# Performance work log

Measured on AMD Instinct MI355X. Metric: run time of the kernel, lower is better.

Reference implementation:

```python
import jax, jax.numpy as jnp
import numpy as np

N_HEAD = 16
ROPE_THETA = 10000.0


def setup_inputs() -> dict:
    key = jax.random.key(0)
    k0, k1, k2 = jax.random.split(key, 3)
    B, T, C = 2, 2048, 1024
    s = 0.02  # GPT-2 style init scale
    return {
        "x": jax.random.normal(k0, (B, T, C), jnp.float32),
        "w_attn": jax.random.normal(k1, (C, 3 * C), jnp.float32) * s,
        "b_attn": jnp.zeros((3 * C,), jnp.float32),
        "w_proj": jax.random.normal(k2, (C, C), jnp.float32) * s,
        "b_proj": jnp.zeros((C,), jnp.float32),
    }


def _rope(x):
    # x: [B, H, T, D]; interleaved-pair rotary (lucidrains rotate_queries_or_keys)
    T, D = x.shape[-2], x.shape[-1]
    inv_freq = 1.0 / (ROPE_THETA ** (jnp.arange(0, D, 2, dtype=jnp.float32) / D))
    freqs = jnp.arange(T, dtype=jnp.float32)[:, None] * inv_freq[None, :]  # [T, D/2]
    emb = jnp.repeat(freqs, 2, axis=-1)  # [T, D], each freq duplicated per pair
    cos, sin = jnp.cos(emb), jnp.sin(emb)
    xr = x.reshape(*x.shape[:-1], D // 2, 2)
    x1, x2 = xr[..., 0], xr[..., 1]
    rot = jnp.stack((-x2, x1), axis=-1).reshape(x.shape)  # rotate_half
    return x * cos + rot * sin


def reference(x, w_attn, b_attn, w_proj, b_proj):
    B, T, C = x.shape
    H = N_HEAD
    D = C // H
    qkv = x @ w_attn + b_attn                      # [B, T, 3C]
    q, k, v = jnp.split(qkv, 3, axis=-1)

    def heads(t):
        return t.reshape(B, T, H, D).transpose(0, 2, 1, 3)  # [B, H, T, D]

    q, k, v = heads(q), heads(k), heads(v)
    q = _rope(q)
    k = _rope(k)

    att = jnp.einsum("bhqd,bhkd->bhqk", q, k) * (1.0 / np.sqrt(D))
    causal = jnp.tril(jnp.ones((T, T), dtype=bool))
    att = jnp.where(causal, att, -jnp.inf)
    att = jax.nn.softmax(att, axis=-1)
    y = jnp.einsum("bhqk,bhkd->bhqd", att, v)
    y = y.transpose(0, 2, 1, 3).reshape(B, T, C)
    return y @ w_proj + b_proj
```

## Files before the change

### kernel.cpp

```cpp
#include <hip/hip_runtime.h>
#include <hip/hip_bf16.h>
#include <stdint.h>

typedef __hip_bfloat16 bf16;
typedef __attribute__((ext_vector_type(8))) short bf16x8;
typedef __attribute__((ext_vector_type(4))) float f32x4;

__device__ inline float bf2f(bf16 v) { return __bfloat162float(v); }
__device__ inline bf16 f2bf(float f) { return __float2bfloat16(f); }

__device__ inline void glds16(const void* g, void* l) {
    __builtin_amdgcn_global_load_lds(
        (const __attribute__((address_space(1))) uint32_t*)g,
        (__attribute__((address_space(3))) uint32_t*)l, 16, 0, 0);
}

__global__ __launch_bounds__(256) void conv_x(const float* __restrict__ in,
                                              bf16* __restrict__ out)
{
    size_t i = ((size_t)blockIdx.x * 256 + threadIdx.x) * 8;
    float4 f0 = *(const float4*)(in + i);
    float4 f1 = *(const float4*)(in + i + 4);
    union { bf16x8 v; bf16 e[8]; } u;
    u.e[0] = f2bf(f0.x); u.e[1] = f2bf(f0.y); u.e[2] = f2bf(f0.z); u.e[3] = f2bf(f0.w);
    u.e[4] = f2bf(f1.x); u.e[5] = f2bf(f1.y); u.e[6] = f2bf(f1.z); u.e[7] = f2bf(f1.w);
    *(bf16x8*)(out + i) = u.v;
}

__global__ __launch_bounds__(256) void conv_wt(const float* __restrict__ W,
                                               bf16* __restrict__ Wt, int N, int K)
{
    __shared__ bf16 t[64][72];
    const int n0 = blockIdx.x * 64, k0 = blockIdx.y * 64;
    const int tid = threadIdx.x;
#pragma unroll
    for (int p = 0; p < 4; ++p) {
        int idx = p * 256 + tid;
        int kr = idx >> 4, c4 = idx & 15;
        float4 f = *(const float4*)(W + (size_t)(k0 + kr) * N + n0 + c4 * 4);
        t[kr][c4 * 4 + 0] = f2bf(f.x); t[kr][c4 * 4 + 1] = f2bf(f.y);
        t[kr][c4 * 4 + 2] = f2bf(f.z); t[kr][c4 * 4 + 3] = f2bf(f.w);
    }
    __syncthreads();
#pragma unroll
    for (int p = 0; p < 2; ++p) {
        int idx = p * 256 + tid;
        int nr = idx >> 3, ch = idx & 7;
        union { bf16x8 v; bf16 e[8]; } u;
#pragma unroll
        for (int j = 0; j < 8; ++j) u.e[j] = t[ch * 8 + j][nr];
        *(bf16x8*)(Wt + (size_t)(n0 + nr) * K + k0 + ch * 8) = u.v;
    }
}

template <bool OUTF32>
__global__ __launch_bounds__(256) void gemm_bt(
    const bf16* __restrict__ A, const bf16* __restrict__ Bt,
    const float* __restrict__ bias, int M, int N, int K, void* __restrict__ outv)
{
    __shared__ __align__(16) bf16 sa[128 * 32];
    __shared__ __align__(16) bf16 sb[128 * 32];

    const int tid  = threadIdx.x;
    const int wave = tid >> 6, lane = tid & 63;
    const int quad = lane >> 4, l16 = lane & 15;
    const int wm = wave >> 1, wn = wave & 1;
    const int row0 = blockIdx.x * 128, n0 = blockIdx.y * 128;

    f32x4 acc[4][4] = {};

    const int sm = wave * 16 + (lane >> 2);
    const int sk = (lane & 3) * 8;
    const bf16* ga = A  + (size_t)(row0 + sm) * K + sk;
    const bf16* gb = Bt + (size_t)(n0  + sm) * K + sk;
    bf16* la = sa + wave * 512;
    bf16* lb = sb + wave * 512;

    for (int k0 = 0; k0 < K; k0 += 32) {
        __syncthreads();
        glds16(ga + k0, la);
        glds16(ga + k0 + (size_t)64 * K, la + 2048);
        glds16(gb + k0, lb);
        glds16(gb + k0 + (size_t)64 * K, lb + 2048);
        __syncthreads();

        bf16x8 af[4], bfr[4];
#pragma unroll
        for (int mi = 0; mi < 4; ++mi)
            af[mi] = *(const bf16x8*)&sa[(wm * 64 + mi * 16 + l16) * 32 + quad * 8];
#pragma unroll
        for (int ni = 0; ni < 4; ++ni)
            bfr[ni] = *(const bf16x8*)&sb[(wn * 64 + ni * 16 + l16) * 32 + quad * 8];
#pragma unroll
        for (int mi = 0; mi < 4; ++mi)
#pragma unroll
            for (int ni = 0; ni < 4; ++ni)
                acc[mi][ni] = __builtin_amdgcn_mfma_f32_16x16x32_bf16(
                    af[mi], bfr[ni], acc[mi][ni], 0, 0, 0);
    }

#pragma unroll
    for (int ni = 0; ni < 4; ++ni) {
        int col = n0 + wn * 64 + ni * 16 + l16;
        float bvv = bias[col];
#pragma unroll
        for (int mi = 0; mi < 4; ++mi) {
#pragma unroll
            for (int r = 0; r < 4; ++r) {
                int row = row0 + wm * 64 + mi * 16 + quad * 4 + r;
                float v = acc[mi][ni][r] + bvv;
                if (OUTF32) ((float*)outv)[(size_t)row * N + col] = v;
                else        ((bf16*)outv)[(size_t)row * N + col] = f2bf(v);
            }
        }
    }
}

__global__ __launch_bounds__(256) void rope_k(
    const bf16* __restrict__ qkv, bf16* __restrict__ q, bf16* __restrict__ k)
{
    int gid = blockIdx.x * 256 + threadIdx.x;
    int p  = gid & 31, d0 = p * 2;
    int t  = (gid >> 5) & 2047;
    int h  = (gid >> 16) & 15;
    int b  = gid >> 20;

    size_t src = ((size_t)(b * 2048 + t)) * 3072 + h * 64 + d0;
    size_t dst = (((size_t)(b * 16 + h)) * 2048 + t) * 64 + d0;

    float invf = expf(-(float)d0 * (9.210340371976184f / 64.0f));
    float sn, cs;
    sincosf((float)t * invf, &sn, &cs);

    float q0 = bf2f(qkv[src]),        q1 = bf2f(qkv[src + 1]);
    float k0 = bf2f(qkv[src + 1024]), k1 = bf2f(qkv[src + 1025]);
    q[dst]     = f2bf((q0 * cs - q1 * sn) * 0.125f);
    q[dst + 1] = f2bf((q1 * cs + q0 * sn) * 0.125f);
    k[dst]     = f2bf(k0 * cs - k1 * sn);
    k[dst + 1] = f2bf(k1 * cs + k0 * sn);
}

__global__ __launch_bounds__(256) void transpose_v(
    const bf16* __restrict__ qkv, bf16* __restrict__ vt)
{
    __shared__ bf16 t[64][72];
    const int t0 = blockIdx.x * 64;
    const int bh = blockIdx.y, b = bh >> 4, h = bh & 15;
    const int tid = threadIdx.x;
#pragma unroll
    for (int p = 0; p < 2; ++p) {
        int idx = p * 256 + tid;
        int tr = idx >> 3, ch = idx & 7;
        bf16x8 v = *(const bf16x8*)(qkv + ((size_t)(b * 2048 + t0 + tr)) * 3072
                                    + 2048 + h * 64 + ch * 8);
#pragma unroll
        for (int j = 0; j < 8; ++j) t[tr][ch * 8 + j] = ((const bf16*)&v)[j];
    }
    __syncthreads();
#pragma unroll
    for (int p = 0; p < 2; ++p) {
        int idx = p * 256 + tid;
        int dr = idx >> 3, ch = idx & 7;
        union { bf16x8 v; bf16 e[8]; } u;
#pragma unroll
        for (int j = 0; j < 8; ++j) u.e[j] = t[ch * 8 + j][dr];
        *(bf16x8*)(vt + ((size_t)bh * 64 + dr) * 2048 + t0 + ch * 8) = u.v;
    }
}

__global__ __launch_bounds__(256) void attn_k(
    const bf16* __restrict__ qg, const bf16* __restrict__ kg,
    const bf16* __restrict__ vtg, bf16* __restrict__ y)
{
    __shared__ __align__(16) bf16 sK[128 * 64];
    __shared__ __align__(16) bf16 sV[64 * 128];
    __shared__ __align__(16) bf16 pL[4][16][136];

    const int tid  = threadIdx.x;
    const int wave = tid >> 6, lane = tid & 63;
    const int quad = lane >> 4, l16 = lane & 15;
    const int bh   = blockIdx.x;
    const int pair = blockIdx.y;
    const bf16* Q  = qg  + (size_t)bh * 2048 * 64;
    const bf16* K  = kg  + (size_t)bh * 2048 * 64;
    const bf16* Vt = vtg + (size_t)bh * 64 * 2048;
    const int b = bh >> 4, h = bh & 15;

    for (int half = 0; half < 2; ++half) {
        const int qt = half ? (31 - pair) : pair;
        const int q0 = qt * 64 + wave * 16;

        bf16x8 aq[2];
        aq[0] = *(const bf16x8*)(Q + (size_t)(q0 + l16) * 64 + quad * 8);
        aq[1] = *(const bf16x8*)(Q + (size_t)(q0 + l16) * 64 + 32 + quad * 8);

        f32x4 o[4] = {};
        float m_r[4] = {-1e30f, -1e30f, -1e30f, -1e30f};
        float l_r[4] = {0.f, 0.f, 0.f, 0.f};

        for (int kt = 0; kt <= q0 + 15; kt += 128) {
            __syncthreads();
#pragma unroll
            for (int c = 0; c < 4; ++c) {
                int key = wave * 32 + c * 8 + (lane >> 3);
                int p = lane & 7;
                glds16(K + (size_t)(kt + key) * 64 + ((p ^ key) & 7) * 8,
                       &sK[(wave * 32 + c * 8) * 64]);
            }
#pragma unroll
            for (int c = 0; c < 4; ++c) {
                int d = wave * 16 + c * 4 + (lane >> 4);
                int p = lane & 15;
                glds16(Vt + (size_t)d * 2048 + kt + ((p ^ d) & 15) * 8,
                       &sV[(wave * 16 + c * 4) * 128]);
            }
            __syncthreads();

            const int nlast = min(7, (q0 - kt) >> 4);
            f32x4 sc[8];
#pragma unroll
            for (int nt = 0; nt < 8; ++nt) {
                if (nt > nlast) continue;
                int key = nt * 16 + l16;
                f32x4 s0 = {};
                bf16x8 bk0 = *(const bf16x8*)&sK[key * 64 + ((quad ^ key) & 7) * 8];
                s0 = __builtin_amdgcn_mfma_f32_16x16x32_bf16(aq[0], bk0, s0, 0, 0, 0);
                bf16x8 bk1 = *(const bf16x8*)&sK[key * 64 + (((4 + quad) ^ key) & 7) * 8];
                sc[nt] = __builtin_amdgcn_mfma_f32_16x16x32_bf16(aq[1], bk1, s0, 0, 0, 0);
            }
            {
                const int diag = (q0 - kt) >> 4;
                if (diag <= 7) {
                    int key = kt + diag * 16 + l16;
#pragma unroll
                    for (int r = 0; r < 4; ++r) {
                        int row = q0 + quad * 4 + r;
                        if (key > row) sc[diag][r] = -1e30f;
                    }
                }
            }
            float rowmax[4] = {-1e30f, -1e30f, -1e30f, -1e30f};
#pragma unroll
            for (int nt = 0; nt < 8; ++nt) {
                if (nt > nlast) continue;
#pragma unroll
                for (int r = 0; r < 4; ++r) rowmax[r] = fmaxf(rowmax[r], sc[nt][r]);
            }
#pragma unroll
            for (int off = 1; off < 16; off <<= 1)
#pragma unroll
                for (int r = 0; r < 4; ++r)
                    rowmax[r] = fmaxf(rowmax[r], __shfl_xor(rowmax[r], off));

            float alpha[4];
#pragma unroll
            for (int r = 0; r < 4; ++r) {
                float mn = fmaxf(m_r[r], rowmax[r]);
                alpha[r] = __expf(m_r[r] - mn);
                m_r[r] = mn;
            }
            float rs[4] = {0.f, 0.f, 0.f, 0.f};
#pragma unroll
            for (int nt = 0; nt < 8; ++nt) {
                if (nt > nlast) continue;
#pragma unroll
                for (int r = 0; r < 4; ++r) {
                    float p = __expf(sc[nt][r] - m_r[r]);
                    sc[nt][r] = p;
                    rs[r] += p;
                }
            }
#pragma unroll
            for (int off = 1; off < 16; off <<= 1)
#pragma unroll
                for (int r = 0; r < 4; ++r) rs[r] += __shfl_xor(rs[r], off);
#pragma unroll
            for (int r = 0; r < 4; ++r) l_r[r] = l_r[r] * alpha[r] + rs[r];
#pragma unroll
            for (int nt = 0; nt < 4; ++nt)
#pragma unroll
                for (int r = 0; r < 4; ++r) o[nt][r] *= alpha[r];

#pragma unroll
            for (int nt = 0; nt < 8; ++nt) {
                if (nt > nlast) continue;
                int blk = (2 * nt + (l16 >> 3)) ^ quad;
#pragma unroll
                for (int r = 0; r < 4; ++r)
                    pL[wave][quad * 4 + r][blk * 8 + (l16 & 7)] = f2bf(sc[nt][r]);
            }
            if (nlast < 7 && !(nlast & 1)) {
                int blk = (2 * (nlast + 1) + (l16 >> 3)) ^ quad;
#pragma unroll
                for (int r = 0; r < 4; ++r)
                    pL[wave][quad * 4 + r][blk * 8 + (l16 & 7)] = f2bf(0.f);
            }
#pragma unroll
            for (int c = 0; c < 4; ++c) {
                if (c > (nlast >> 1)) continue;
                bf16x8 pa = *(const bf16x8*)&pL[wave][l16][(((4 * c + quad) ^ (l16 >> 2)) * 8)];
#pragma unroll
                for (int dnt = 0; dnt < 4; ++dnt) {
                    int d = dnt * 16 + l16;
                    int cc = c * 4 + quad;
                    bf16x8 vb = *(const bf16x8*)&sV[d * 128 + ((cc ^ d) & 15) * 8];
                    o[dnt] = __builtin_amdgcn_mfma_f32_16x16x32_bf16(pa, vb, o[dnt], 0, 0, 0);
                }
            }
        }

#pragma unroll
        for (int r = 0; r < 4; ++r) {
            float inv = 1.0f / l_r[r];
            int qq = q0 + quad * 4 + r;
#pragma unroll
            for (int nt = 0; nt < 4; ++nt) {
                int d = nt * 16 + l16;
                y[((size_t)(b * 2048 + qq)) * 1024 + h * 64 + d] = f2bf(o[nt][r] * inv);
            }
        }
    }
}

extern "C" void kernel_launch(void* const* d_in, const int* in_sizes, int n_in,
                              void* d_out, int out_size, void* d_ws, size_t ws_size,
                              hipStream_t stream) {
    const float* x      = (const float*)d_in[0];
    const float* w_attn = (const float*)d_in[1];
    const float* b_attn = (const float*)d_in[2];
    const float* w_proj = (const float*)d_in[3];
    const float* b_proj = (const float*)d_in[4];
    float* out = (float*)d_out;

    bf16* xbf = (bf16*)d_ws;
    bf16* wat = xbf + (size_t)4194304;
    bf16* wpt = wat + (size_t)3145728;
    bf16* qkv = wpt + (size_t)1048576;
    bf16* qh  = qkv + (size_t)12582912;
    bf16* kh  = qh  + (size_t)4194304;
    bf16* vt  = kh  + (size_t)4194304;
    bf16* yws = vt  + (size_t)4194304;

    dim3 blk(256);
    conv_x<<<dim3(2048), blk, 0, stream>>>(x, xbf);
    conv_wt<<<dim3(48, 16), blk, 0, stream>>>(w_attn, wat, 3072, 1024);
    conv_wt<<<dim3(16, 16), blk, 0, stream>>>(w_proj, wpt, 1024, 1024);
    gemm_bt<false><<<dim3(32, 24), blk, 0, stream>>>(xbf, wat, b_attn,
                                                     4096, 3072, 1024, qkv);
    rope_k<<<dim3(8192), blk, 0, stream>>>(qkv, qh, kh);
    transpose_v<<<dim3(32, 32), blk, 0, stream>>>(qkv, vt);
    attn_k<<<dim3(32, 16), blk, 0, stream>>>(qh, kh, vt, yws);
    gemm_bt<true><<<dim3(32, 8), blk, 0, stream>>>(yws, wpt, b_proj,
                                                   4096, 1024, 1024, out);
    (void)in_sizes; (void)n_in; (void)ws_size; (void)out_size;
}
```

Baseline: 231.7 us.

## Fuse RoPE into QKV GEMM epilogue with precomputed sin/cos table, use exp2

Removes the separate RoPE kernel by applying rotary embedding, the q scale and the head-major scatter directly in the QKV GEMM epilogue. Pair partners are exchanged with a lane shuffle, and cos/sin come from a table built inside the x-conversion kernel. The q scale now folds in log2(e) so attention can use the native exp2 instead of __expf. This drops the full qkv intermediate write and re-read, at the cost of a heavier epilogue with scattered 2-byte stores and table loads.

```diff
diff --git a/kernel.cpp b/kernel.cpp
--- a/kernel.cpp
+++ b/kernel.cpp
@@ -8,6 +8,8 @@
 
 __device__ inline float bf2f(bf16 v) { return __bfloat162float(v); }
 __device__ inline bf16 f2bf(float f) { return __float2bfloat16(f); }
+
+#define QSCALE 0.18033688011112042f
 
 __device__ inline void glds16(const void* g, void* l) {
     __builtin_amdgcn_global_load_lds(
@@ -15,16 +17,26 @@
         (__attribute__((address_space(3))) uint32_t*)l, 16, 0, 0);
 }
 
-__global__ __launch_bounds__(256) void conv_x(const float* __restrict__ in,
-                                              bf16* __restrict__ out)
-{
-    size_t i = ((size_t)blockIdx.x * 256 + threadIdx.x) * 8;
-    float4 f0 = *(const float4*)(in + i);
-    float4 f1 = *(const float4*)(in + i + 4);
-    union { bf16x8 v; bf16 e[8]; } u;
-    u.e[0] = f2bf(f0.x); u.e[1] = f2bf(f0.y); u.e[2] = f2bf(f0.z); u.e[3] = f2bf(f0.w);
-    u.e[4] = f2bf(f1.x); u.e[5] = f2bf(f1.y); u.e[6] = f2bf(f1.z); u.e[7] = f2bf(f1.w);
-    *(bf16x8*)(out + i) = u.v;
+__global__ __launch_bounds__(256) void conv_x_tab(const float* __restrict__ in,
+                                                  bf16* __restrict__ out,
+                                                  float2* __restrict__ tab)
+{
+    if (blockIdx.x < 2048) {
+        size_t i = ((size_t)blockIdx.x * 256 + threadIdx.x) * 8;
+        float4 f0 = *(const float4*)(in + i);
+        float4 f1 = *(const float4*)(in + i + 4);
+        union { bf16x8 v; bf16 e[8]; } u;
+        u.e[0] = f2bf(f0.x); u.e[1] = f2bf(f0.y); u.e[2] = f2bf(f0.z); u.e[3] = f2bf(f0.w);
+        u.e[4] = f2bf(f1.x); u.e[5] = f2bf(f1.y); u.e[6] = f2bf(f1.z); u.e[7] = f2bf(f1.w);
+        *(bf16x8*)(out + i) = u.v;
+    } else {
+        int i = (blockIdx.x - 2048) * 256 + threadIdx.x;
+        int t = i >> 5, p = i & 31;
+        float invf = expf(-(float)(2 * p) * (9.210340371976184f / 64.0f));
+        float sn, cs;
+        sincosf((float)t * invf, &sn, &cs);
+        tab[i] = make_float2(cs, sn);
+    }
 }
 
 __global__ __launch_bounds__(256) void conv_wt(const float* __restrict__ W,
@@ -53,10 +65,12 @@
     }
 }
 
-template <bool OUTF32>
+template <int MODE>
 __global__ __launch_bounds__(256) void gemm_bt(
     const bf16* __restrict__ A, const bf16* __restrict__ Bt,
-    const float* __restrict__ bias, int M, int N, int K, void* __restrict__ outv)
+    const float* __restrict__ bias, int M, int N, int K,
+    void* __restrict__ o1, bf16* __restrict__ o2, bf16* __restrict__ o3,
+    const float2* __restrict__ tab)
 {
     __shared__ __align__(16) bf16 sa[128 * 32];
     __shared__ __align__(16) bf16 sb[128 * 32];
@@ -99,60 +113,63 @@
                     af[mi], bfr[ni], acc[mi][ni], 0, 0, 0);
     }
 
-#pragma unroll
-    for (int ni = 0; ni < 4; ++ni) {
-        int col = n0 + wn * 64 + ni * 16 + l16;
-        float bvv = bias[col];
-#pragma unroll
-        for (int mi = 0; mi < 4; ++mi) {
-#pragma unroll
-            for (int r = 0; r < 4; ++r) {
-                int row = row0 + wm * 64 + mi * 16 + quad * 4 + r;
-                float v = acc[mi][ni][r] + bvv;
-                if (OUTF32) ((float*)outv)[(size_t)row * N + col] = v;
-                else        ((bf16*)outv)[(size_t)row * N + col] = f2bf(v);
-            }
+    if (MODE == 1) {
+#pragma unroll
+        for (int ni = 0; ni < 4; ++ni) {
+            int col = n0 + wn * 64 + ni * 16 + l16;
+            float bvv = bias[col];
+#pragma unroll
+            for (int mi = 0; mi < 4; ++mi)
+#pragma unroll
+                for (int r = 0; r < 4; ++r) {
+                    int row = row0 + wm * 64 + mi * 16 + quad * 4 + r;
+                    ((float*)o1)[(size_t)row * N + col] = acc[mi][ni][r] + bvv;
+                }
         }
-    }
-}
-
-__global__ __launch_bounds__(256) void rope_k(
-    const bf16* __restrict__ qkv, bf16* __restrict__ q, bf16* __restrict__ k)
-{
-    int gid = blockIdx.x * 256 + threadIdx.x;
-    int p  = gid & 31, d0 = p * 2;
-    int t  = (gid >> 5) & 2047;
-    int h  = (gid >> 16) & 15;
-    int b  = gid >> 20;
-
-    size_t src = ((size_t)(b * 2048 + t)) * 3072 + h * 64 + d0;
-    size_t dst = (((size_t)(b * 16 + h)) * 2048 + t) * 64 + d0;
-
-    float invf = expf(-(float)d0 * (9.210340371976184f / 64.0f));
-    float sn, cs;
-    sincosf((float)t * invf, &sn, &cs);
-
-    float q0 = bf2f(qkv[src]),        q1 = bf2f(qkv[src + 1]);
-    float k0 = bf2f(qkv[src + 1024]), k1 = bf2f(qkv[src + 1025]);
-    q[dst]     = f2bf((q0 * cs - q1 * sn) * 0.125f);
-    q[dst + 1] = f2bf((q1 * cs + q0 * sn) * 0.125f);
-    k[dst]     = f2bf(k0 * cs - k1 * sn);
-    k[dst + 1] = f2bf(k1 * cs + k0 * sn);
+    } else {
+        const int which = n0 >> 10;
+        const int h = ((n0 & 1023) >> 6) + wn;
+        bf16* dst = (which == 0) ? (bf16*)o1 : (which == 1) ? o2 : o3;
+#pragma unroll
+        for (int ni = 0; ni < 4; ++ni) {
+            int col = n0 + wn * 64 + ni * 16 + l16;
+            int d = ni * 16 + l16;
+            float bvv = bias[col];
+#pragma unroll
+            for (int mi = 0; mi < 4; ++mi)
+#pragma unroll
+                for (int r = 0; r < 4; ++r) {
+                    int row = row0 + wm * 64 + mi * 16 + quad * 4 + r;
+                    int b = row >> 11, t = row & 2047;
+                    float v = acc[mi][ni][r] + bvv;
+                    float outv;
+                    if (which == 2) {
+                        outv = v;
+                    } else {
+                        float vp = __shfl_xor(v, 1);
+                        float2 cs = tab[t * 32 + (d >> 1)];
+                        outv = (d & 1) ? (v * cs.x + vp * cs.y)
+                                       : (v * cs.x - vp * cs.y);
+                        if (which == 0) outv *= QSCALE;
+                    }
+                    dst[(((size_t)(b * 16 + h)) * 2048 + t) * 64 + d] = f2bf(outv);
+                }
+        }
+    }
 }
 
 __global__ __launch_bounds__(256) void transpose_v(
-    const bf16* __restrict__ qkv, bf16* __restrict__ vt)
+    const bf16* __restrict__ vh, bf16* __restrict__ vt)
 {
     __shared__ bf16 t[64][72];
     const int t0 = blockIdx.x * 64;
-    const int bh = blockIdx.y, b = bh >> 4, h = bh & 15;
+    const int bh = blockIdx.y;
     const int tid = threadIdx.x;
 #pragma unroll
     for (int p = 0; p < 2; ++p) {
         int idx = p * 256 + tid;
         int tr = idx >> 3, ch = idx & 7;
-        bf16x8 v = *(const bf16x8*)(qkv + ((size_t)(b * 2048 + t0 + tr)) * 3072
-                                    + 2048 + h * 64 + ch * 8);
+        bf16x8 v = *(const bf16x8*)(vh + ((size_t)bh * 2048 + t0 + tr) * 64 + ch * 8);
 #pragma unroll
         for (int j = 0; j < 8; ++j) t[tr][ch * 8 + j] = ((const bf16*)&v)[j];
     }
@@ -256,7 +273,7 @@
 #pragma unroll
             for (int r = 0; r < 4; ++r) {
                 float mn = fmaxf(m_r[r], rowmax[r]);
-                alpha[r] = __expf(m_r[r] - mn);
+                alpha[r] = __builtin_amdgcn_exp2f(m_r[r] - mn);
                 m_r[r] = mn;
             }
             float rs[4] = {0.f, 0.f, 0.f, 0.f};
@@ -265,7 +282,7 @@
                 if (nt > nlast) continue;
 #pragma unroll
                 for (int r = 0; r < 4; ++r) {
-                    float p = __expf(sc[nt][r] - m_r[r]);
+                    float p = __builtin_amdgcn_exp2f(sc[nt][r] - m_r[r]);
                     sc[nt][r] = p;
                     rs[r] += p;
                 }
@@ -335,22 +352,22 @@
     bf16* xbf = (bf16*)d_ws;
     bf16* wat = xbf + (size_t)4194304;
     bf16* wpt = wat + (size_t)3145728;
-    bf16* qkv = wpt + (size_t)1048576;
-    bf16* qh  = qkv + (size_t)12582912;
+    bf16* qh  = wpt + (size_t)1048576;
     bf16* kh  = qh  + (size_t)4194304;
-    bf16* vt  = kh  + (size_t)4194304;
+    bf16* vh  = kh  + (size_t)4194304;
+    bf16* vt  = vh  + (size_t)4194304;
     bf16* yws = vt  + (size_t)4194304;
+    float2* tab = (float2*)(yws + (size_t)4194304);
 
     dim3 blk(256);
-    conv_x<<<dim3(2048), blk, 0, stream>>>(x, xbf);
+    conv_x_tab<<<dim3(2304), blk, 0, stream>>>(x, xbf, tab);
     conv_wt<<<dim3(48, 16), blk, 0, stream>>>(w_attn, wat, 3072, 1024);
     conv_wt<<<dim3(16, 16), blk, 0, stream>>>(w_proj, wpt, 1024, 1024);
-    gemm_bt<false><<<dim3(32, 24), blk, 0, stream>>>(xbf, wat, b_attn,
-                                                     4096, 3072, 1024, qkv);
-    rope_k<<<dim3(8192), blk, 0, stream>>>(qkv, qh, kh);
-    transpose_v<<<dim3(32, 32), blk, 0, stream>>>(qkv, vt);
+    gemm_bt<2><<<dim3(32, 24), blk, 0, stream>>>(xbf, wat, b_attn, 4096, 3072, 1024,
+                                                 qh, kh, vh, tab);
+    transpose_v<<<dim3(32, 32), blk, 0, stream>>>(vh, vt);
     attn_k<<<dim3(32, 16), blk, 0, stream>>>(qh, kh, vt, yws);
-    gemm_bt<true><<<dim3(32, 8), blk, 0, stream>>>(yws, wpt, b_proj,
-                                                   4096, 1024, 1024, out);
+    gemm_bt<1><<<dim3(32, 8), blk, 0, stream>>>(yws, wpt, b_proj, 4096, 1024, 1024,
+                                                out, nullptr, nullptr, nullptr);
     (void)in_sizes; (void)n_in; (void)ws_size; (void)out_size;
 }
```

Result: slower. 249.9 us (+7.8%).

## Double-buffer 64-key K/V tiles in attention and precompute RoPE table

Applied to the files above, without the earlier changes.

The attention kernel drops from 128-key tiles loaded synchronously to 64-key tiles with double buffering, so the next tile's async global-to-LDS load is issued while the current tile is computed. Q is pre-scaled by log2(e)/sqrt(D) so the softmax can use the native exp2 instead of __expf. The RoPE cos/sin values move into a precomputed table built alongside the x conversion, removing sincos from rope_k. Smaller tiles mean more iterations and barriers, and the single barrier per iteration has to order correctly with the async LDS loads.

```diff
diff --git a/kernel.cpp b/kernel.cpp
--- a/kernel.cpp
+++ b/kernel.cpp
@@ -8,6 +8,8 @@
 
 __device__ inline float bf2f(bf16 v) { return __bfloat162float(v); }
 __device__ inline bf16 f2bf(float f) { return __float2bfloat16(f); }
+
+#define QSCALE 0.18033688011112042f
 
 __device__ inline void glds16(const void* g, void* l) {
     __builtin_amdgcn_global_load_lds(
@@ -15,16 +17,26 @@
         (__attribute__((address_space(3))) uint32_t*)l, 16, 0, 0);
 }
 
-__global__ __launch_bounds__(256) void conv_x(const float* __restrict__ in,
-                                              bf16* __restrict__ out)
-{
-    size_t i = ((size_t)blockIdx.x * 256 + threadIdx.x) * 8;
-    float4 f0 = *(const float4*)(in + i);
-    float4 f1 = *(const float4*)(in + i + 4);
-    union { bf16x8 v; bf16 e[8]; } u;
-    u.e[0] = f2bf(f0.x); u.e[1] = f2bf(f0.y); u.e[2] = f2bf(f0.z); u.e[3] = f2bf(f0.w);
-    u.e[4] = f2bf(f1.x); u.e[5] = f2bf(f1.y); u.e[6] = f2bf(f1.z); u.e[7] = f2bf(f1.w);
-    *(bf16x8*)(out + i) = u.v;
+__global__ __launch_bounds__(256) void conv_x_tab(const float* __restrict__ in,
+                                                  bf16* __restrict__ out,
+                                                  float2* __restrict__ tab)
+{
+    if (blockIdx.x < 2048) {
+        size_t i = ((size_t)blockIdx.x * 256 + threadIdx.x) * 8;
+        float4 f0 = *(const float4*)(in + i);
+        float4 f1 = *(const float4*)(in + i + 4);
+        union { bf16x8 v; bf16 e[8]; } u;
+        u.e[0] = f2bf(f0.x); u.e[1] = f2bf(f0.y); u.e[2] = f2bf(f0.z); u.e[3] = f2bf(f0.w);
+        u.e[4] = f2bf(f1.x); u.e[5] = f2bf(f1.y); u.e[6] = f2bf(f1.z); u.e[7] = f2bf(f1.w);
+        *(bf16x8*)(out + i) = u.v;
+    } else {
+        int i = (blockIdx.x - 2048) * 256 + threadIdx.x;
+        int t = i >> 5, p = i & 31;
+        float invf = expf(-(float)(2 * p) * (9.210340371976184f / 64.0f));
+        float sn, cs;
+        sincosf((float)t * invf, &sn, &cs);
+        tab[i] = make_float2(cs, sn);
+    }
 }
 
 __global__ __launch_bounds__(256) void conv_wt(const float* __restrict__ W,
@@ -104,7 +116,7 @@
         int col = n0 + wn * 64 + ni * 16 + l16;
         float bvv = bias[col];
 #pragma unroll
-        for (int mi = 0; mi < 4; ++mi) {
+        for (int mi = 0; mi < 4; ++mi)
 #pragma unroll
             for (int r = 0; r < 4; ++r) {
                 int row = row0 + wm * 64 + mi * 16 + quad * 4 + r;
@@ -112,12 +124,12 @@
                 if (OUTF32) ((float*)outv)[(size_t)row * N + col] = v;
                 else        ((bf16*)outv)[(size_t)row * N + col] = f2bf(v);
             }
-        }
     }
 }
 
 __global__ __launch_bounds__(256) void rope_k(
-    const bf16* __restrict__ qkv, bf16* __restrict__ q, bf16* __restrict__ k)
+    const bf16* __restrict__ qkv, bf16* __restrict__ q, bf16* __restrict__ k,
+    const float2* __restrict__ tab)
 {
     int gid = blockIdx.x * 256 + threadIdx.x;
     int p  = gid & 31, d0 = p * 2;
@@ -128,16 +140,13 @@
     size_t src = ((size_t)(b * 2048 + t)) * 3072 + h * 64 + d0;
     size_t dst = (((size_t)(b * 16 + h)) * 2048 + t) * 64 + d0;
 
-    float invf = expf(-(float)d0 * (9.210340371976184f / 64.0f));
-    float sn, cs;
-    sincosf((float)t * invf, &sn, &cs);
-
+    float2 cs = tab[t * 32 + p];
     float q0 = bf2f(qkv[src]),        q1 = bf2f(qkv[src + 1]);
     float k0 = bf2f(qkv[src + 1024]), k1 = bf2f(qkv[src + 1025]);
-    q[dst]     = f2bf((q0 * cs - q1 * sn) * 0.125f);
-    q[dst + 1] = f2bf((q1 * cs + q0 * sn) * 0.125f);
-    k[dst]     = f2bf(k0 * cs - k1 * sn);
-    k[dst + 1] = f2bf(k1 * cs + k0 * sn);
+    q[dst]     = f2bf((q0 * cs.x - q1 * cs.y) * QSCALE);
+    q[dst + 1] = f2bf((q1 * cs.x + q0 * cs.y) * QSCALE);
+    k[dst]     = f2bf(k0 * cs.x - k1 * cs.y);
+    k[dst + 1] = f2bf(k1 * cs.x + k0 * cs.y);
 }
 
 __global__ __launch_bounds__(256) void transpose_v(
@@ -172,9 +181,9 @@
     const bf16* __restrict__ qg, const bf16* __restrict__ kg,
     const bf16* __restrict__ vtg, bf16* __restrict__ y)
 {
-    __shared__ __align__(16) bf16 sK[128 * 64];
-    __shared__ __align__(16) bf16 sV[64 * 128];
-    __shared__ __align__(16) bf16 pL[4][16][136];
+    __shared__ __align__(16) bf16 sK[2][64 * 64];
+    __shared__ __align__(16) bf16 sV[2][64 * 64];
+    __shared__ __align__(16) bf16 pL[4][16][72];
 
     const int tid  = threadIdx.x;
     const int wave = tid >> 6, lane = tid & 63;
@@ -186,6 +195,9 @@
     const bf16* Vt = vtg + (size_t)bh * 64 * 2048;
     const int b = bh >> 4, h = bh & 15;
 
+    const int srow = wave * 16 + (lane >> 3);
+    const int sp   = lane & 7;
+
     for (int half = 0; half < 2; ++half) {
         const int qt = half ? (31 - pair) : pair;
         const int q0 = qt * 64 + wave * 16;
@@ -198,39 +210,49 @@
         float m_r[4] = {-1e30f, -1e30f, -1e30f, -1e30f};
         float l_r[4] = {0.f, 0.f, 0.f, 0.f};
 
-        for (int kt = 0; kt <= q0 + 15; kt += 128) {
+        const int nIter = qt + 1;
+
+        __syncthreads();
+#pragma unroll
+        for (int c = 0; c < 2; ++c) {
+            int row = srow + c * 8;
+            glds16(K + (size_t)row * 64 + ((sp ^ row) & 7) * 8,
+                   &sK[0][(wave * 16 + c * 8) * 64]);
+            glds16(Vt + (size_t)row * 2048 + ((sp ^ row) & 7) * 8,
+                   &sV[0][(wave * 16 + c * 8) * 64]);
+        }
+
+        for (int it = 0; it < nIter; ++it) {
+            const int kt = it * 64;
+            const int buf = it & 1;
             __syncthreads();
-#pragma unroll
-            for (int c = 0; c < 4; ++c) {
-                int key = wave * 32 + c * 8 + (lane >> 3);
-                int p = lane & 7;
-                glds16(K + (size_t)(kt + key) * 64 + ((p ^ key) & 7) * 8,
-                       &sK[(wave * 32 + c * 8) * 64]);
-            }
-#pragma unroll
-            for (int c = 0; c < 4; ++c) {
-                int d = wave * 16 + c * 4 + (lane >> 4);
-                int p = lane & 15;
-                glds16(Vt + (size_t)d * 2048 + kt + ((p ^ d) & 15) * 8,
-                       &sV[(wave * 16 + c * 4) * 128]);
-            }
-            __syncthreads();
-
-            const int nlast = min(7, (q0 - kt) >> 4);
-            f32x4 sc[8];
-#pragma unroll
-            for (int nt = 0; nt < 8; ++nt) {
+            if (it + 1 < nIter) {
+                const int ktn = kt + 64;
+#pragma unroll
+                for (int c = 0; c < 2; ++c) {
+                    int row = srow + c * 8;
+                    glds16(K + (size_t)(ktn + row) * 64 + ((sp ^ row) & 7) * 8,
+                           &sK[buf ^ 1][(wave * 16 + c * 8) * 64]);
+                    glds16(Vt + (size_t)row * 2048 + ktn + ((sp ^ row) & 7) * 8,
+                           &sV[buf ^ 1][(wave * 16 + c * 8) * 64]);
+                }
+            }
+
+            const int nlast = min(3, (q0 - kt) >> 4);
+            f32x4 sc[4];
+#pragma unroll
+            for (int nt = 0; nt < 4; ++nt) {
                 if (nt > nlast) continue;
                 int key = nt * 16 + l16;
                 f32x4 s0 = {};
-                bf16x8 bk0 = *(const bf16x8*)&sK[key * 64 + ((quad ^ key) & 7) * 8];
+                bf16x8 bk0 = *(const bf16x8*)&sK[buf][key * 64 + ((quad ^ key) & 7) * 8];
                 s0 = __builtin_amdgcn_mfma_f32_16x16x32_bf16(aq[0], bk0, s0, 0, 0, 0);
-                bf16x8 bk1 = *(const bf16x8*)&sK[key * 64 + (((4 + quad) ^ key) & 7) * 8];
+                bf16x8 bk1 = *(const bf16x8*)&sK[buf][key * 64 + (((4 + quad) ^ key) & 7) * 8];
                 sc[nt] = __builtin_amdgcn_mfma_f32_16x16x32_bf16(aq[1], bk1, s0, 0, 0, 0);
             }
             {
                 const int diag = (q0 - kt) >> 4;
-                if (diag <= 7) {
+                if (diag <= 3) {
                     int key = kt + diag * 16 + l16;
 #pragma unroll
                     for (int r = 0; r < 4; ++r) {
@@ -241,7 +263,7 @@
             }
             float rowmax[4] = {-1e30f, -1e30f, -1e30f, -1e30f};
 #pragma unroll
-            for (int nt = 0; nt < 8; ++nt) {
+            for (int nt = 0; nt < 4; ++nt) {
                 if (nt > nlast) continue;
 #pragma unroll
                 for (int r = 0; r < 4; ++r) rowmax[r] = fmaxf(rowmax[r], sc[nt][r]);
@@ -256,16 +278,16 @@
 #pragma unroll
             for (int r = 0; r < 4; ++r) {
                 float mn = fmaxf(m_r[r], rowmax[r]);
-                alpha[r] = __expf(m_r[r] - mn);
+                alpha[r] = __builtin_amdgcn_exp2f(m_r[r] - mn);
                 m_r[r] = mn;
             }
             float rs[4] = {0.f, 0.f, 0.f, 0.f};
 #pragma unroll
-            for (int nt = 0; nt < 8; ++nt) {
+            for (int nt = 0; nt < 4; ++nt) {
                 if (nt > nlast) continue;
 #pragma unroll
                 for (int r = 0; r < 4; ++r) {
-                    float p = __expf(sc[nt][r] - m_r[r]);
+                    float p = __builtin_amdgcn_exp2f(sc[nt][r] - m_r[r]);
                     sc[nt][r] = p;
                     rs[r] += p;
                 }
@@ -282,28 +304,28 @@
                 for (int r = 0; r < 4; ++r) o[nt][r] *= alpha[r];
 
 #pragma unroll
-            for (int nt = 0; nt < 8; ++nt) {
+            for (int nt = 0; nt < 4; ++nt) {
                 if (nt > nlast) continue;
                 int blk = (2 * nt + (l16 >> 3)) ^ quad;
 #pragma unroll
                 for (int r = 0; r < 4; ++r)
                     pL[wave][quad * 4 + r][blk * 8 + (l16 & 7)] = f2bf(sc[nt][r]);
             }
-            if (nlast < 7 && !(nlast & 1)) {
+            if (nlast < 3 && !(nlast & 1)) {
                 int blk = (2 * (nlast + 1) + (l16 >> 3)) ^ quad;
 #pragma unroll
                 for (int r = 0; r < 4; ++r)
                     pL[wave][quad * 4 + r][blk * 8 + (l16 & 7)] = f2bf(0.f);
             }
 #pragma unroll
-            for (int c = 0; c < 4; ++c) {
+            for (int c = 0; c < 2; ++c) {
                 if (c > (nlast >> 1)) continue;
                 bf16x8 pa = *(const bf16x8*)&pL[wave][l16][(((4 * c + quad) ^ (l16 >> 2)) * 8)];
 #pragma unroll
                 for (int dnt = 0; dnt < 4; ++dnt) {
                     int d = dnt * 16 + l16;
                     int cc = c * 4 + quad;
-                    bf16x8 vb = *(const bf16x8*)&sV[d * 128 + ((cc ^ d) & 15) * 8];
+                    bf16x8 vb = *(const bf16x8*)&sV[buf][d * 64 + ((cc ^ d) & 7) * 8];
                     o[dnt] = __builtin_amdgcn_mfma_f32_16x16x32_bf16(pa, vb, o[dnt], 0, 0, 0);
                 }
             }
@@ -340,14 +362,15 @@
     bf16* kh  = qh  + (size_t)4194304;
     bf16* vt  = kh  + (size_t)4194304;
     bf16* yws = vt  + (size_t)4194304;
+    float2* tab = (float2*)(yws + (size_t)4194304);
 
     dim3 blk(256);
-    conv_x<<<dim3(2048), blk, 0, stream>>>(x, xbf);
+    conv_x_tab<<<dim3(2304), blk, 0, stream>>>(x, xbf, tab);
     conv_wt<<<dim3(48, 16), blk, 0, stream>>>(w_attn, wat, 3072, 1024);
     conv_wt<<<dim3(16, 16), blk, 0, stream>>>(w_proj, wpt, 1024, 1024);
     gemm_bt<false><<<dim3(32, 24), blk, 0, stream>>>(xbf, wat, b_attn,
                                                      4096, 3072, 1024, qkv);
-    rope_k<<<dim3(8192), blk, 0, stream>>>(qkv, qh, kh);
+    rope_k<<<dim3(8192), blk, 0, stream>>>(qkv, qh, kh, tab);
     transpose_v<<<dim3(32, 32), blk, 0, stream>>>(qkv, vt);
     attn_k<<<dim3(32, 16), blk, 0, stream>>>(qh, kh, vt, yws);
     gemm_bt<true><<<dim3(32, 8), blk, 0, stream>>>(yws, wpt, b_proj,
```

Result: slower. 245.3 us (+5.9%).
